# Kernel tuning notes

Measured on AMD Instinct MI355X. Metric: run time of the kernel, lower is better.

The kernel has to match this reference:

```python
import jax, jax.numpy as jnp
import numpy as np

N = 50000      # num_nodes
E = 800000     # num_edges (avg degree 16)
IN, HID, OUT = 128, 64, 64


def setup_inputs() -> dict:
    key = jax.random.key(0)
    ks = jax.random.split(key, 4)
    x = jax.random.normal(ks[0], (N, IN), dtype=jnp.float32)
    edge_index = jax.random.randint(ks[1], (2, E), 0, N, dtype=jnp.int32)
    # GCNConv params: weight [in, out] and bias [out] per layer
    W1 = jax.random.normal(ks[2], (IN, HID), dtype=jnp.float32) * 0.05
    b1 = jnp.zeros((HID,), dtype=jnp.float32)
    W2 = jax.random.normal(ks[3], (HID, OUT), dtype=jnp.float32) * 0.05
    b2 = jnp.zeros((OUT,), dtype=jnp.float32)
    return {"x": x, "edge_index": edge_index, "W1": W1, "b1": b1, "W2": W2, "b2": b2}


def _gcn_conv(x, W, b, src, dst, norm, n):
    # linear transform, then normalized gather->scatter-add aggregation
    h = x @ W                                    # [N, out]
    msg = h[src] * norm[:, None]                 # [E+N, out] gathered messages
    out = jax.ops.segment_sum(msg, dst, num_segments=n)
    return out + b


def reference(x, edge_index, W1, b1, W2, b2):
    n = x.shape[0]
    # add self-loops (PyG GCNConv default)
    loop = jnp.arange(n, dtype=edge_index.dtype)
    src = jnp.concatenate([edge_index[0], loop])
    dst = jnp.concatenate([edge_index[1], loop])
    # symmetric normalization D^-1/2 A D^-1/2 (degree over destination)
    deg = jax.ops.segment_sum(jnp.ones_like(dst, dtype=x.dtype), dst, num_segments=n)
    dinv = jnp.where(deg > 0, jax.lax.rsqrt(deg), jnp.zeros_like(deg))
    norm = dinv[src] * dinv[dst]                 # [E+N]
    h = _gcn_conv(x, W1, b1, src, dst, norm, n)
    h = jax.nn.leaky_relu(h, negative_slope=0.01)
    # dropout is identity in eval mode (training=False)
    return _gcn_conv(h, W2, b2, src, dst, norm, n)
```

## Files before the change

### kernel.cpp

```cpp
#include <hip/hip_runtime.h>
#include <hip/hip_fp16.h>


#define NBC   128
#define BSH   7
#define NBMAX 512

typedef __bf16 bf16x8 __attribute__((ext_vector_type(8)));
typedef float  f32x4  __attribute__((ext_vector_type(4)));

__device__ __forceinline__ unsigned short f2bf(float f) {
    unsigned u = __float_as_uint(f);
    unsigned r = u + 0x7fff + ((u >> 16) & 1);
    return (unsigned short)(r >> 16);
}
__device__ __forceinline__ float bf2f(unsigned short h) {
    return __uint_as_float(((unsigned)h) << 16);
}

__global__ __launch_bounds__(256) void k_hist1(const int* __restrict__ dst,
                                               int* __restrict__ T, int E, int nbuck) {
    __shared__ int hist[NBMAX];
    for (int i = threadIdx.x; i < nbuck; i += 256) hist[i] = 0;
    __syncthreads();
    const int per = (E + NBC - 1) / NBC;
    const int beg = blockIdx.x * per, end = min(beg + per, E);
    for (int i = beg + threadIdx.x; i < end; i += 256)
        atomicAdd(&hist[dst[i] >> BSH], 1);
    __syncthreads();
    for (int b = threadIdx.x; b < nbuck; b += 256)
        T[b * NBC + blockIdx.x] = hist[b];
}

__global__ __launch_bounds__(1024) void k_bsum(const int* __restrict__ in,
                                               int* __restrict__ bsum, int m) {
    __shared__ int red[16];
    const int t = threadIdx.x;
    const int i = blockIdx.x * 1024 + t;
    int v = (i < m) ? in[i] : 0;
#pragma unroll
    for (int o = 32; o; o >>= 1) v += __shfl_down(v, o);
    if ((t & 63) == 0) red[t >> 6] = v;
    __syncthreads();
    if (t == 0) {
        int s = 0;
#pragma unroll
        for (int w = 0; w < 16; ++w) s += red[w];
        bsum[blockIdx.x] = s;
    }
}

__global__ void k_sbsum(const int* __restrict__ bsum, int* __restrict__ boff, int nb) {
    if (threadIdx.x == 0 && blockIdx.x == 0) {
        int run = 0;
        for (int i = 0; i < nb; ++i) { boff[i] = run; run += bsum[i]; }
    }
}

__global__ __launch_bounds__(1024) void k_scanexc(
    const int* __restrict__ in, const int* __restrict__ boff,
    int* __restrict__ out, int m) {
    __shared__ int sh[1024];
    const int t = threadIdx.x;
    const int i = blockIdx.x * 1024 + t;
    const int v = (i < m) ? in[i] : 0;
    sh[t] = v;
    __syncthreads();
#pragma unroll
    for (int o = 1; o < 1024; o <<= 1) {
        int add = (t >= o) ? sh[t - o] : 0;
        __syncthreads();
        sh[t] += add;
        __syncthreads();
    }
    if (i < m) out[i] = boff[blockIdx.x] + sh[t] - v;
}

__global__ __launch_bounds__(256) void k_part1(
    const int* __restrict__ src, const int* __restrict__ dst,
    const int* __restrict__ Toff, unsigned* __restrict__ stage, int E, int nbuck) {
    __shared__ int base[NBMAX];
    __shared__ int cnt[NBMAX];
    for (int i = threadIdx.x; i < nbuck; i += 256) {
        base[i] = Toff[i * NBC + blockIdx.x];
        cnt[i] = 0;
    }
    __syncthreads();
    const int per = (E + NBC - 1) / NBC;
    const int beg = blockIdx.x * per, end = min(beg + per, E);
    for (int i = beg + threadIdx.x; i < end; i += 256) {
        int d = dst[i], s = src[i];
        int b = d >> BSH;
        int p = atomicAdd(&cnt[b], 1);
        stage[base[b] + p] = ((unsigned)(d & 127) << 17) | (unsigned)s;
    }
}

__global__ __launch_bounds__(256) void k_part2(
    const int* __restrict__ Toff, const unsigned* __restrict__ stage,
    int* __restrict__ csr, int* __restrict__ rowptr, float* __restrict__ dinv,
    int n, int E, int nbuck) {
    __shared__ int cnt[128], sc[128], curs[128];
    __shared__ int rbs, res;
    const int t = threadIdx.x;
    const int b = blockIdx.x;
    if (t < 128) cnt[t] = 0;
    if (t == 0) {
        rbs = Toff[b * NBC];
        res = (b == nbuck - 1) ? E : Toff[(b + 1) * NBC];
    }
    __syncthreads();
    const int rb = rbs, re = res;
    for (int i = rb + t; i < re; i += 256)
        atomicAdd(&cnt[(stage[i] >> 17) & 127], 1);
    __syncthreads();
    if (t < 128) sc[t] = cnt[t];
    __syncthreads();
#pragma unroll
    for (int o = 1; o < 128; o <<= 1) {
        int add = (t < 128 && t >= o) ? sc[t - o] : 0;
        __syncthreads();
        if (t < 128) sc[t] += add;
        __syncthreads();
    }
    if (t < 128) {
        const int excl = rb + sc[t] - cnt[t];
        curs[t] = excl;
        const int gi = b * 128 + t;
        if (gi < n) {
            rowptr[gi] = excl;
            dinv[gi] = rsqrtf((float)cnt[t] + 1.f);
            if (gi == n - 1) rowptr[n] = rb + sc[t];
        }
    }
    __syncthreads();
    for (int i = rb + t; i < re; i += 256) {
        unsigned r = stage[i];
        int p = atomicAdd(&curs[(r >> 17) & 127], 1);
        csr[p] = (int)(r & 0x1FFFF);
    }
}

__global__ void k_wsplit(const float* __restrict__ W, unsigned short* __restrict__ out, int K) {
    int i = blockIdx.x * blockDim.x + threadIdx.x;
    if (i >= K * 64) return;
    int k = i >> 6, c = i & 63;
    float v = W[k * 64 + c];
    unsigned short hi = f2bf(v);
    unsigned short lo = f2bf(v - bf2f(hi));
    int T = K / 32;
    int t = k >> 5, kk = k & 31, g = kk >> 3, j = kk & 7;
    int ct = c >> 4, lane = g * 16 + (c & 15);
    out[(((size_t)(0 * T + t) * 4 + ct) * 64 + lane) * 8 + j] = hi;
    out[(((size_t)(1 * T + t) * 4 + ct) * 64 + lane) * 8 + j] = lo;
}

template<int K, bool LEAKY>
__global__ __launch_bounds__(256) void k_gemm_mfma(
    const float* __restrict__ A, const unsigned short* __restrict__ Ws,
    const float* __restrict__ dinv, __half* __restrict__ C, int n) {
    constexpr int T = K / 32;
    const int lane = threadIdx.x & 63;
    const int w = blockIdx.x * 4 + (threadIdx.x >> 6);
    const int r0 = w * 16;
    if (r0 >= n) return;
    const int g = lane >> 4, rA = lane & 15;

    bf16x8 ahi[T], alo[T];
    const float* arow = A + (size_t)(r0 + rA) * K + g * 8;
#pragma unroll
    for (int t = 0; t < T; ++t) {
        float4 v0 = *(const float4*)(arow + t * 32);
        float4 v1 = *(const float4*)(arow + t * 32 + 4);
        float f[8] = {v0.x, v0.y, v0.z, v0.w, v1.x, v1.y, v1.z, v1.w};
        union { unsigned short u[8]; bf16x8 v; } H, L;
#pragma unroll
        for (int j = 0; j < 8; ++j) {
            float x = f[j];
            if (LEAKY) x = x > 0.f ? x : 0.01f * x;
            unsigned short h = f2bf(x);
            H.u[j] = h;
            L.u[j] = f2bf(x - bf2f(h));
        }
        ahi[t] = H.v; alo[t] = L.v;
    }

    f32x4 acc[4];
#pragma unroll
    for (int ct = 0; ct < 4; ++ct) acc[ct] = (f32x4){0.f, 0.f, 0.f, 0.f};

#pragma unroll
    for (int ct = 0; ct < 4; ++ct) {
#pragma unroll
        for (int t = 0; t < T; ++t) {
            union { uint4 q; bf16x8 v; } Bh, Bl;
            Bh.q = *(const uint4*)(Ws + (((size_t)(0 * T + t) * 4 + ct) * 64 + lane) * 8);
            Bl.q = *(const uint4*)(Ws + (((size_t)(1 * T + t) * 4 + ct) * 64 + lane) * 8);
            acc[ct] = __builtin_amdgcn_mfma_f32_16x16x32_bf16(ahi[t], Bh.v, acc[ct], 0, 0, 0);
            acc[ct] = __builtin_amdgcn_mfma_f32_16x16x32_bf16(ahi[t], Bl.v, acc[ct], 0, 0, 0);
            acc[ct] = __builtin_amdgcn_mfma_f32_16x16x32_bf16(alo[t], Bh.v, acc[ct], 0, 0, 0);
        }
    }

    float dv[4];
#pragma unroll
    for (int r = 0; r < 4; ++r) dv[r] = dinv[r0 + g * 4 + r];

    __half* crow = C + (size_t)(r0 + g * 4) * 64 + rA;
#pragma unroll
    for (int ct = 0; ct < 4; ++ct)
#pragma unroll
        for (int r = 0; r < 4; ++r)
            crow[(size_t)r * 64 + ct * 16] = __float2half_rn(acc[ct][r] * dv[r]);
}

__global__ __launch_bounds__(256) void k_aggcsr(
    const int* __restrict__ rowptr, const int* __restrict__ csr,
    const float* __restrict__ dinv, const __half* __restrict__ hs,
    const float* __restrict__ bias, float* __restrict__ out, int n) {
    const int lane = threadIdx.x & 63;
    const int wid  = blockIdx.x * 4 + (threadIdx.x >> 6);
    const int nw   = gridDim.x * 4;
    const float bl = bias[lane];
    for (int dd = wid; dd < n; dd += nw) {
        const int d = __builtin_amdgcn_readfirstlane(dd);
        const int beg = rowptr[d], end = rowptr[d + 1];
        float a0 = 0.f, a1 = 0.f, a2 = 0.f, a3 = 0.f;
        float a4 = 0.f, a5 = 0.f, a6 = 0.f, a7 = 0.f;
        int j = beg;
        for (; j + 8 <= end; j += 8) {
            int s0 = csr[j + 0], s1 = csr[j + 1], s2 = csr[j + 2], s3 = csr[j + 3];
            int s4 = csr[j + 4], s5 = csr[j + 5], s6 = csr[j + 6], s7 = csr[j + 7];
            a0 += __half2float(hs[(size_t)s0 * 64 + lane]);
            a1 += __half2float(hs[(size_t)s1 * 64 + lane]);
            a2 += __half2float(hs[(size_t)s2 * 64 + lane]);
            a3 += __half2float(hs[(size_t)s3 * 64 + lane]);
            a4 += __half2float(hs[(size_t)s4 * 64 + lane]);
            a5 += __half2float(hs[(size_t)s5 * 64 + lane]);
            a6 += __half2float(hs[(size_t)s6 * 64 + lane]);
            a7 += __half2float(hs[(size_t)s7 * 64 + lane]);
        }
        for (; j < end; ++j)
            a0 += __half2float(hs[(size_t)csr[j] * 64 + lane]);
        const float di = dinv[d];
        const float acc = ((a0 + a1) + (a2 + a3)) + ((a4 + a5) + (a6 + a7));
        out[(size_t)d * 64 + lane] =
            (acc + __half2float(hs[(size_t)d * 64 + lane])) * di + bl;
    }
}

extern "C" void kernel_launch(void* const* d_in, const int* in_sizes, int n_in,
                              void* d_out, int out_size, void* d_ws, size_t ws_size,
                              hipStream_t stream) {
    const float* x  = (const float*)d_in[0];
    const int*   ei = (const int*)d_in[1];
    const float* W1 = (const float*)d_in[2];
    const float* b1 = (const float*)d_in[3];
    const float* W2 = (const float*)d_in[4];
    const float* b2 = (const float*)d_in[5];
    float* out = (float*)d_out;

    const int n = in_sizes[0] / 128;
    const int E = in_sizes[1] / 2;
    const int* src = ei;
    const int* dst = ei + E;

    const int nbuck = (n + 127) >> BSH;
    const int m = nbuck * NBC;
    const int nb2 = (m + 1023) / 1024;

    char* ws = (char*)d_ws;
    size_t off = 0;
    auto alloc = [&](size_t bytes) { void* p = ws + off; off = (off + bytes + 255) & ~(size_t)255; return p; };
    int*      T      = (int*)alloc((size_t)m * 4);
    int*      Toff   = (int*)alloc((size_t)m * 4);
    int*      bsum   = (int*)alloc((size_t)nb2 * 4);
    int*      boff   = (int*)alloc((size_t)nb2 * 4);
    unsigned* stage  = (unsigned*)alloc((size_t)E * 4);
    int*      csr    = (int*)alloc((size_t)E * 4);
    int*      rowptr = (int*)alloc((size_t)(n + 1) * 4);
    float*    dinv   = (float*)alloc((size_t)n * 4);
    __half*   hs     = (__half*)alloc((size_t)n * 64 * 2);
    float*    out1   = (float*)alloc((size_t)n * 64 * 4);
    unsigned short* W1s = (unsigned short*)alloc((size_t)2 * 128 * 64 * 2);
    unsigned short* W2s = (unsigned short*)alloc((size_t)2 * 64 * 64 * 2);
    (void)ws_size; (void)n_in; (void)out_size;

    k_hist1  <<<NBC, 256, 0, stream>>>(dst, T, E, nbuck);
    k_bsum   <<<nb2, 1024, 0, stream>>>(T, bsum, m);
    k_sbsum  <<<1, 64, 0, stream>>>(bsum, boff, nb2);
    k_scanexc<<<nb2, 1024, 0, stream>>>(T, boff, Toff, m);
    k_part1  <<<NBC, 256, 0, stream>>>(src, dst, Toff, stage, E, nbuck);
    k_part2  <<<nbuck, 256, 0, stream>>>(Toff, stage, csr, rowptr, dinv, n, E, nbuck);

    k_wsplit <<<(128 * 64 + 255) / 256, 256, 0, stream>>>(W1, W1s, 128);
    k_wsplit <<<(64 * 64 + 255) / 256, 256, 0, stream>>>(W2, W2s, 64);

    const int gemmBlocks = (n / 16 + 3) / 4;
    k_gemm_mfma<128, false><<<gemmBlocks, 256, 0, stream>>>(x, W1s, dinv, hs, n);
    k_aggcsr<<<2048, 256, 0, stream>>>(rowptr, csr, dinv, hs, b1, out1, n);

    k_gemm_mfma<64, true><<<gemmBlocks, 256, 0, stream>>>(out1, W2s, dinv, hs, n);
    k_aggcsr<<<2048, 256, 0, stream>>>(rowptr, csr, dinv, hs, b2, out, n);
}
```

Before: 115.3 us.

## Sort CSR buckets in LDS, store layer-1 output as fp16, merge weight split kernels

k_part2 now stages each bucket's edges in shared memory, counting-sorts them there, and writes the csr segment contiguously instead of scattering to global memory, with the old global path kept as a fallback for oversized buckets. The intermediate layer-1 aggregation output is stored as fp16 instead of fp32, which halves its write and its read by the second GEMM at some precision cost. The two weight-split launches are merged into one kernel to save a launch.

```diff
diff --git a/kernel.cpp b/kernel.cpp
--- a/kernel.cpp
+++ b/kernel.cpp
@@ -1,10 +1,12 @@
 #include <hip/hip_runtime.h>
 #include <hip/hip_fp16.h>
+#include <type_traits>
 
 
 #define NBC   128
 #define BSH   7
 #define NBMAX 512
+#define CAP   8192
 
 typedef __bf16 bf16x8 __attribute__((ext_vector_type(8)));
 typedef float  f32x4  __attribute__((ext_vector_type(4)));
@@ -100,6 +102,8 @@
     const int* __restrict__ Toff, const unsigned* __restrict__ stage,
     int* __restrict__ csr, int* __restrict__ rowptr, float* __restrict__ dinv,
     int n, int E, int nbuck) {
+    __shared__ unsigned buf[CAP];
+    __shared__ unsigned srt[CAP];
     __shared__ int cnt[128], sc[128], curs[128];
     __shared__ int rbs, res;
     const int t = threadIdx.x;
@@ -110,41 +114,79 @@
         res = (b == nbuck - 1) ? E : Toff[(b + 1) * NBC];
     }
     __syncthreads();
-    const int rb = rbs, re = res;
-    for (int i = rb + t; i < re; i += 256)
-        atomicAdd(&cnt[(stage[i] >> 17) & 127], 1);
-    __syncthreads();
-    if (t < 128) sc[t] = cnt[t];
-    __syncthreads();
-#pragma unroll
-    for (int o = 1; o < 128; o <<= 1) {
-        int add = (t < 128 && t >= o) ? sc[t - o] : 0;
-        __syncthreads();
-        if (t < 128) sc[t] += add;
-        __syncthreads();
-    }
-    if (t < 128) {
-        const int excl = rb + sc[t] - cnt[t];
-        curs[t] = excl;
-        const int gi = b * 128 + t;
-        if (gi < n) {
-            rowptr[gi] = excl;
-            dinv[gi] = rsqrtf((float)cnt[t] + 1.f);
-            if (gi == n - 1) rowptr[n] = rb + sc[t];
-        }
-    }
-    __syncthreads();
-    for (int i = rb + t; i < re; i += 256) {
-        unsigned r = stage[i];
-        int p = atomicAdd(&curs[(r >> 17) & 127], 1);
-        csr[p] = (int)(r & 0x1FFFF);
-    }
-}
-
-__global__ void k_wsplit(const float* __restrict__ W, unsigned short* __restrict__ out, int K) {
+    const int rb = rbs, re = res, len = re - rb;
+    if (len <= CAP) {
+        for (int i = t; i < len; i += 256) {
+            unsigned r = stage[rb + i];
+            buf[i] = r;
+            atomicAdd(&cnt[(r >> 17) & 127], 1);
+        }
+        __syncthreads();
+        if (t < 128) sc[t] = cnt[t];
+        __syncthreads();
+#pragma unroll
+        for (int o = 1; o < 128; o <<= 1) {
+            int add = (t < 128 && t >= o) ? sc[t - o] : 0;
+            __syncthreads();
+            if (t < 128) sc[t] += add;
+            __syncthreads();
+        }
+        if (t < 128) {
+            curs[t] = sc[t] - cnt[t];
+            const int gi = b * 128 + t;
+            if (gi < n) {
+                rowptr[gi] = rb + sc[t] - cnt[t];
+                dinv[gi] = rsqrtf((float)cnt[t] + 1.f);
+                if (gi == n - 1) rowptr[n] = rb + sc[t];
+            }
+        }
+        __syncthreads();
+        for (int i = t; i < len; i += 256) {
+            unsigned r = buf[i];
+            int p = atomicAdd(&curs[(r >> 17) & 127], 1);
+            srt[p] = r & 0x1FFFF;
+        }
+        __syncthreads();
+        for (int i = t; i < len; i += 256) csr[rb + i] = (int)srt[i];
+    } else {
+        for (int i = rb + t; i < re; i += 256)
+            atomicAdd(&cnt[(stage[i] >> 17) & 127], 1);
+        __syncthreads();
+        if (t < 128) sc[t] = cnt[t];
+        __syncthreads();
+#pragma unroll
+        for (int o = 1; o < 128; o <<= 1) {
+            int add = (t < 128 && t >= o) ? sc[t - o] : 0;
+            __syncthreads();
+            if (t < 128) sc[t] += add;
+            __syncthreads();
+        }
+        if (t < 128) {
+            curs[t] = rb + sc[t] - cnt[t];
+            const int gi = b * 128 + t;
+            if (gi < n) {
+                rowptr[gi] = rb + sc[t] - cnt[t];
+                dinv[gi] = rsqrtf((float)cnt[t] + 1.f);
+                if (gi == n - 1) rowptr[n] = rb + sc[t];
+            }
+        }
+        __syncthreads();
+        for (int i = rb + t; i < re; i += 256) {
+            unsigned r = stage[i];
+            int p = atomicAdd(&curs[(r >> 17) & 127], 1);
+            csr[p] = (int)(r & 0x1FFFF);
+        }
+    }
+}
+
+__global__ void k_wsplit2(const float* __restrict__ W1, const float* __restrict__ W2,
+                          unsigned short* __restrict__ W1s, unsigned short* __restrict__ W2s) {
     int i = blockIdx.x * blockDim.x + threadIdx.x;
-    if (i >= K * 64) return;
-    int k = i >> 6, c = i & 63;
+    const float* W; unsigned short* out; int K, idx;
+    if (i < 128 * 64)            { W = W1; out = W1s; K = 128; idx = i; }
+    else if (i < 128 * 64 + 64 * 64) { W = W2; out = W2s; K = 64; idx = i - 128 * 64; }
+    else return;
+    int k = idx >> 6, c = idx & 63;
     float v = W[k * 64 + c];
     unsigned short hi = f2bf(v);
     unsigned short lo = f2bf(v - bf2f(hi));
@@ -155,9 +197,9 @@
     out[(((size_t)(1 * T + t) * 4 + ct) * 64 + lane) * 8 + j] = lo;
 }
 
-template<int K, bool LEAKY>
+template<int K, bool LEAKY, typename AT>
 __global__ __launch_bounds__(256) void k_gemm_mfma(
-    const float* __restrict__ A, const unsigned short* __restrict__ Ws,
+    const AT* __restrict__ A, const unsigned short* __restrict__ Ws,
     const float* __restrict__ dinv, __half* __restrict__ C, int n) {
     constexpr int T = K / 32;
     const int lane = threadIdx.x & 63;
@@ -167,12 +209,21 @@
     const int g = lane >> 4, rA = lane & 15;
 
     bf16x8 ahi[T], alo[T];
-    const float* arow = A + (size_t)(r0 + rA) * K + g * 8;
+    const AT* arow = A + (size_t)(r0 + rA) * K + g * 8;
 #pragma unroll
     for (int t = 0; t < T; ++t) {
-        float4 v0 = *(const float4*)(arow + t * 32);
-        float4 v1 = *(const float4*)(arow + t * 32 + 4);
-        float f[8] = {v0.x, v0.y, v0.z, v0.w, v1.x, v1.y, v1.z, v1.w};
+        float f[8];
+        if constexpr (std::is_same<AT, float>::value) {
+            float4 v0 = *(const float4*)(arow + t * 32);
+            float4 v1 = *(const float4*)(arow + t * 32 + 4);
+            f[0] = v0.x; f[1] = v0.y; f[2] = v0.z; f[3] = v0.w;
+            f[4] = v1.x; f[5] = v1.y; f[6] = v1.z; f[7] = v1.w;
+        } else {
+            union { uint4 q; __half h[8]; } u;
+            u.q = *(const uint4*)(arow + t * 32);
+#pragma unroll
+            for (int j = 0; j < 8; ++j) f[j] = __half2float(u.h[j]);
+        }
         union { unsigned short u[8]; bf16x8 v; } H, L;
 #pragma unroll
         for (int j = 0; j < 8; ++j) {
@@ -214,10 +265,11 @@
             crow[(size_t)r * 64 + ct * 16] = __float2half_rn(acc[ct][r] * dv[r]);
 }
 
+template<typename OT>
 __global__ __launch_bounds__(256) void k_aggcsr(
     const int* __restrict__ rowptr, const int* __restrict__ csr,
     const float* __restrict__ dinv, const __half* __restrict__ hs,
-    const float* __restrict__ bias, float* __restrict__ out, int n) {
+    const float* __restrict__ bias, OT* __restrict__ out, int n) {
     const int lane = threadIdx.x & 63;
     const int wid  = blockIdx.x * 4 + (threadIdx.x >> 6);
     const int nw   = gridDim.x * 4;
@@ -244,8 +296,11 @@
             a0 += __half2float(hs[(size_t)csr[j] * 64 + lane]);
         const float di = dinv[d];
         const float acc = ((a0 + a1) + (a2 + a3)) + ((a4 + a5) + (a6 + a7));
-        out[(size_t)d * 64 + lane] =
-            (acc + __half2float(hs[(size_t)d * 64 + lane])) * di + bl;
+        const float v = (acc + __half2float(hs[(size_t)d * 64 + lane])) * di + bl;
+        if constexpr (std::is_same<OT, __half>::value)
+            out[(size_t)d * 64 + lane] = __float2half_rn(v);
+        else
+            out[(size_t)d * 64 + lane] = v;
     }
 }
 
@@ -281,7 +336,7 @@
     int*      rowptr = (int*)alloc((size_t)(n + 1) * 4);
     float*    dinv   = (float*)alloc((size_t)n * 4);
     __half*   hs     = (__half*)alloc((size_t)n * 64 * 2);
-    float*    out1   = (float*)alloc((size_t)n * 64 * 4);
+    __half*   out1   = (__half*)alloc((size_t)n * 64 * 2);
     unsigned short* W1s = (unsigned short*)alloc((size_t)2 * 128 * 64 * 2);
     unsigned short* W2s = (unsigned short*)alloc((size_t)2 * 64 * 64 * 2);
     (void)ws_size; (void)n_in; (void)out_size;
@@ -293,13 +348,12 @@
     k_part1  <<<NBC, 256, 0, stream>>>(src, dst, Toff, stage, E, nbuck);
     k_part2  <<<nbuck, 256, 0, stream>>>(Toff, stage, csr, rowptr, dinv, n, E, nbuck);
 
-    k_wsplit <<<(128 * 64 + 255) / 256, 256, 0, stream>>>(W1, W1s, 128);
-    k_wsplit <<<(64 * 64 + 255) / 256, 256, 0, stream>>>(W2, W2s, 64);
+    k_wsplit2<<<(128 * 64 + 64 * 64 + 255) / 256, 256, 0, stream>>>(W1, W2, W1s, W2s);
 
     const int gemmBlocks = (n / 16 + 3) / 4;
-    k_gemm_mfma<128, false><<<gemmBlocks, 256, 0, stream>>>(x, W1s, dinv, hs, n);
-    k_aggcsr<<<2048, 256, 0, stream>>>(rowptr, csr, dinv, hs, b1, out1, n);
-
-    k_gemm_mfma<64, true><<<gemmBlocks, 256, 0, stream>>>(out1, W2s, dinv, hs, n);
-    k_aggcsr<<<2048, 256, 0, stream>>>(rowptr, csr, dinv, hs, b2, out, n);
-}
+    k_gemm_mfma<128, false, float><<<gemmBlocks, 256, 0, stream>>>(x, W1s, dinv, hs, n);
+    k_aggcsr<__half><<<2048, 256, 0, stream>>>(rowptr, csr, dinv, hs, b1, out1, n);
+
+    k_gemm_mfma<64, true, __half><<<gemmBlocks, 256, 0, stream>>>(out1, W2s, dinv, hs, n);
+    k_aggcsr<float><<<2048, 256, 0, stream>>>(rowptr, csr, dinv, hs, b2, out, n);
+}
```

Result: faster. 111.3 us (-3.5%).
